# Kernel tuning notes

Measured on AMD Instinct MI355X. Metric: run time of the kernel, lower is better.

Reference implementation:

```python
import jax, jax.numpy as jnp
import numpy as np

N = 100000   # nodes
E = 250000   # directed edges
D = 300      # emb_dim
L = 5        # num_layers
BN_EPS = 1e-5
NUM_ATOM_TYPE, NUM_CHIRALITY_TAG = 120, 3
NUM_BOND_TYPE, NUM_BOND_DIR = 6, 3
SELF_LOOP_BOND = 4


def setup_inputs() -> dict:
    key = jax.random.key(0)
    ks = jax.random.split(key, 14)
    s = 0.02
    x = jnp.stack([jax.random.randint(ks[0], (N,), 0, NUM_ATOM_TYPE),
                   jax.random.randint(ks[1], (N,), 0, NUM_CHIRALITY_TAG)], axis=1)
    edge_index = jax.random.randint(ks[2], (2, E), 0, N)
    edge_attr = jnp.stack([jax.random.randint(ks[3], (E,), 0, 4),  # real bond types 0..3
                           jax.random.randint(ks[4], (E,), 0, NUM_BOND_DIR)], axis=1)
    x_emb1 = jax.random.normal(ks[5], (NUM_ATOM_TYPE, D), jnp.float32) * s
    x_emb2 = jax.random.normal(ks[6], (NUM_CHIRALITY_TAG, D), jnp.float32) * s
    ee1 = jax.random.normal(ks[7], (L, NUM_BOND_TYPE, D), jnp.float32) * s
    ee2 = jax.random.normal(ks[8], (L, NUM_BOND_DIR, D), jnp.float32) * s
    W1 = jax.random.normal(ks[9], (L, D, 2 * D), jnp.float32) * (1.0 / np.sqrt(D))
    b1 = jnp.zeros((L, 2 * D), jnp.float32)
    W2 = jax.random.normal(ks[10], (L, 2 * D, D), jnp.float32) * (1.0 / np.sqrt(2 * D))
    b2 = jnp.zeros((L, D), jnp.float32)
    eps = jnp.zeros((L,), jnp.float32)
    gamma = jnp.ones((L, D), jnp.float32)
    beta = jnp.zeros((L, D), jnp.float32)
    return {"x": x, "edge_index": edge_index, "edge_attr": edge_attr,
            "x_emb1": x_emb1, "x_emb2": x_emb2, "ee1": ee1, "ee2": ee2,
            "W1": W1, "b1": b1, "W2": W2, "b2": b2,
            "eps": eps, "gamma": gamma, "beta": beta}


def reference(x, edge_index, edge_attr, x_emb1, x_emb2, ee1, ee2,
              W1, b1, W2, b2, eps, gamma, beta):
    src, dst = edge_index[0], edge_index[1]
    n = x.shape[0]
    # Input atom embedding
    h = x_emb1[x[:, 0]] + x_emb2[x[:, 1]]  # [N, D]
    for l in range(L):
        # edge embedding gather (real edges)
        e_emb = ee1[l][edge_attr[:, 0]] + ee2[l][edge_attr[:, 1]]  # [E, D]
        # message: x_j + edge_emb, scatter-add to target nodes
        msg = h[src] + e_emb
        aggr = jax.ops.segment_sum(msg, dst, num_segments=n)  # [N, D]
        # self-loop edges: bond_type=4, bond_dir=0; x_j = h_i
        aggr = aggr + h + (ee1[l][SELF_LOOP_BOND] + ee2[l][0])
        # update: mlp((1 + eps) * aggr)
        z = (1.0 + eps[l]) * aggr
        z = jnp.maximum(z @ W1[l] + b1[l], 0.0) @ W2[l] + b2[l]
        # BatchNorm1d (training-mode batch statistics, dropout disabled)
        mean = z.mean(axis=0)
        var = z.var(axis=0)
        h = (z - mean) * jax.lax.rsqrt(var + BN_EPS) * gamma[l] + beta[l]
        if l < L - 1:
            h = jnp.maximum(h, 0.0)
    return h
```

## Files before the change

### kernel.cpp

```cpp
#include <hip/hip_runtime.h>
#include <cstdint>

#define NN 100000
#define NE 250000
#define MP 100096
#define MSTRIP 391
#define SCAN_B 256
#define NBLK ((NN + SCAN_B - 1) / SCAN_B)
#define NSLOT 32

using bf16x8 = __attribute__((ext_vector_type(8))) __bf16;
using f32x4v = __attribute__((ext_vector_type(4))) float;

__device__ __forceinline__ unsigned short f2bf(float f) {
  union { float f; uint32_t u; } v; v.f = f;
  uint32_t r = v.u + 0x7FFFu + ((v.u >> 16) & 1u);
  return (unsigned short)(r >> 16);
}
__device__ __forceinline__ float bf2f(unsigned short u) {
  union { uint32_t u; float f; } v; v.u = ((uint32_t)u) << 16;
  return v.f;
}

__device__ __forceinline__ void ld_lds16(const void* g, void* l) {
  __builtin_amdgcn_global_load_lds(
      (const __attribute__((address_space(1))) void*)g,
      (__attribute__((address_space(3))) void*)l, 16, 0, 0);
}

__global__ void prep_kernel(const float* __restrict__ W1, const float* __restrict__ W2,
                            const float* __restrict__ ee1, const float* __restrict__ ee2,
                            const float* __restrict__ b1, const float* __restrict__ b2, int l,
                            unsigned short* __restrict__ wt1, unsigned short* __restrict__ wt2,
                            float* __restrict__ combo, float* __restrict__ selfv,
                            float* __restrict__ b1p, float* __restrict__ b2p,
                            float* __restrict__ bnsum, float* __restrict__ bnsum2) {
  int i = blockIdx.x * 256 + threadIdx.x;
  if (i < 640 * 320) {
    int n = i / 320, k = i % 320;
    float v = (n < 600 && k < 300) ? W1[(size_t)l * 180000 + k * 600 + n] : 0.f;
    wt1[i] = f2bf(v); return;
  }
  i -= 640 * 320;
  if (i < 384 * 640) {
    int n = i / 640, k = i % 640;
    float v = (n < 300 && k < 600) ? W2[(size_t)l * 180000 + k * 300 + n] : 0.f;
    wt2[i] = f2bf(v); return;
  }
  i -= 384 * 640;
  if (i < 3600) {
    int idx = i / 300, d = i % 300;
    int a = idx / 3, b = idx % 3;
    combo[i] = ee1[l * 1800 + a * 300 + d] + ee2[l * 900 + b * 300 + d]; return;
  }
  i -= 3600;
  if (i < 300) { selfv[i] = ee1[l * 1800 + 4 * 300 + i] + ee2[l * 900 + i]; return; }
  i -= 300;
  if (i < 640) { b1p[i] = (i < 600) ? b1[l * 600 + i] : 0.f; return; }
  i -= 640;
  if (i < 384) { b2p[i] = (i < 300) ? b2[l * 300 + i] : 0.f; return; }
  i -= 384;
  if (i < NSLOT * 384) { bnsum[i] = 0.f; return; }
  i -= NSLOT * 384;
  if (i < NSLOT * 384) { bnsum2[i] = 0.f; return; }
}
#define PREP_TOT (640*320 + 384*640 + 3600 + 300 + 640 + 384 + 2*NSLOT*384)

__global__ void deg_kernel(const int* __restrict__ ei, int* __restrict__ deg) {
  int e = blockIdx.x * 256 + threadIdx.x;
  if (e >= NE) return;
  atomicAdd(&deg[ei[NE + e]], 1);
}

__global__ void scan1_kernel(const int* __restrict__ deg, int* __restrict__ off,
                             int* __restrict__ bsum) {
  __shared__ int tmp[SCAN_B];
  int b = blockIdx.x, t = threadIdx.x;
  int i = b * SCAN_B + t;
  int v = (i < NN) ? deg[i] : 0;
  tmp[t] = v;
  __syncthreads();
  for (int s = 1; s < SCAN_B; s <<= 1) {
    int a = (t >= s) ? tmp[t - s] : 0;
    __syncthreads();
    tmp[t] += a;
    __syncthreads();
  }
  if (i < NN) off[i] = tmp[t] - v;
  if (t == SCAN_B - 1) bsum[b] = tmp[t];
}
__global__ void scan2_kernel(int* __restrict__ bsum) {
  if (threadIdx.x == 0) {
    int acc = 0;
    for (int b = 0; b < NBLK; ++b) { int v = bsum[b]; bsum[b] = acc; acc += v; }
  }
}
__global__ void scan3_kernel(const int* __restrict__ bsum, int* __restrict__ off,
                             int* __restrict__ cursor) {
  int i = blockIdx.x * SCAN_B + threadIdx.x;
  if (i >= NN) return;
  int o = off[i] + bsum[blockIdx.x];
  off[i] = o;
  cursor[i] = o;
}

__global__ void fill_kernel(const int* __restrict__ ei, const int* __restrict__ ea,
                            int* __restrict__ cursor, int* __restrict__ list) {
  int e = blockIdx.x * 256 + threadIdx.x;
  if (e >= NE) return;
  int s = ei[e], d = ei[NE + e];
  int c = ea[2 * e] * 3 + ea[2 * e + 1];
  int p = atomicAdd(&cursor[d], 1);
  list[p] = s * 16 + c;
}

template <int MODE>
__global__ void gather_kernel(const unsigned short* __restrict__ zsrc,
                              const int* __restrict__ x, const float* __restrict__ e1,
                              const float* __restrict__ e2,
                              const float* __restrict__ bnA, const float* __restrict__ bnB,
                              const int* __restrict__ off, const int* __restrict__ deg,
                              const int* __restrict__ list,
                              const float* __restrict__ combo, const float* __restrict__ selfv,
                              const float* __restrict__ eps, int l,
                              unsigned short* __restrict__ abf) {
  int i = blockIdx.x * 256 + threadIdx.x;
  if (i >= NN * 75) return;
  int r = i / 75, q = i % 75;
  float4 a4, b4;
  if (MODE == 1) { a4 = ((const float4*)bnA)[q]; b4 = ((const float4*)bnB)[q]; }

  const ushort4* z4 = (const ushort4*)zsrc;
  const float4* c4 = (const float4*)combo;

  auto loadrow = [&](int s) -> float4 {
    float4 hv;
    if (MODE == 0) {
      float4 u = ((const float4*)(e1 + (size_t)x[2 * s] * 300))[q];
      float4 v = ((const float4*)(e2 + (size_t)x[2 * s + 1] * 300))[q];
      hv.x = u.x + v.x; hv.y = u.y + v.y; hv.z = u.z + v.z; hv.w = u.w + v.w;
    } else {
      ushort4 zv = z4[(size_t)s * 96 + q];
      hv.x = fmaxf(bf2f(zv.x) * a4.x + b4.x, 0.f);
      hv.y = fmaxf(bf2f(zv.y) * a4.y + b4.y, 0.f);
      hv.z = fmaxf(bf2f(zv.z) * a4.z + b4.z, 0.f);
      hv.w = fmaxf(bf2f(zv.w) * a4.w + b4.w, 0.f);
    }
    return hv;
  };

  float4 acc = loadrow(r);
  float4 sv = ((const float4*)selfv)[q];
  acc.x += sv.x; acc.y += sv.y; acc.z += sv.z; acc.w += sv.w;

  int p0 = off[r], dn = deg[r];
  for (int p = 0; p < dn; ++p) {
    int pk = list[p0 + p];
    int s = pk >> 4, c = pk & 15;
    float4 hv = loadrow(s);
    float4 cv = c4[c * 75 + q];
    acc.x += hv.x + cv.x; acc.y += hv.y + cv.y;
    acc.z += hv.z + cv.z; acc.w += hv.w + cv.w;
  }
  float sc = 1.f + eps[l];
  ushort4 o;
  o.x = f2bf(acc.x * sc); o.y = f2bf(acc.y * sc);
  o.z = f2bf(acc.z * sc); o.w = f2bf(acc.w * sc);
  *(ushort4*)(abf + (size_t)r * 320 + q * 4) = o;
}

template <int LDA, int LDB, int NS, int NT, bool RELU, bool OBF16, bool STATS>
__global__ __launch_bounds__(512, 4) void gemm_kernel(
    const unsigned short* __restrict__ A, const unsigned short* __restrict__ B,
    const float* __restrict__ bias, void* __restrict__ C, int K,
    float* __restrict__ bnsum, float* __restrict__ bnsum2) {
  __shared__ unsigned short As[2][256 * 32];
  __shared__ unsigned short Bs[2][128 * 32];
  const int tid = threadIdx.x;
  const int lane = tid & 63;
  const int w = tid >> 6;
  const int wr = w >> 1, wc = w & 1;
  const int l15 = lane & 15, l4 = lane >> 4;

  const int wid = blockIdx.x + gridDim.x * blockIdx.y;
  const int bmi = (wid & 7) + 8 * (wid / (8 * NT));
  const int ny  = (wid >> 3) % NT;
  if (bmi >= MSTRIP) return;
  const int bm = bmi * 256;
  const int bn = ny * 128;

  auto stage = [&](int buf, int kk) {
#pragma unroll
    for (int it = 0; it < 2; ++it) {
      int s = it * 512 + tid;
      int row = s >> 2, kbl = s & 3;
      int kbg = kbl ^ ((row >> 1) & 3);
      ld_lds16(A + (size_t)(bm + row) * LDA + kk + kbg * 8, &As[buf][s * 8]);
    }
    {
      int s = tid;
      int row = s >> 2, kbl = s & 3;
      int kbg = kbl ^ ((row >> 1) & 3);
      ld_lds16(B + (size_t)(bn + row) * LDB + kk + kbg * 8, &Bs[buf][s * 8]);
    }
  };

  f32x4v acc[4][4] = {};
  const int nt = K / 32;

  stage(0, 0);
  for (int t = 0; t < nt; ++t) {
    const int cur = t & 1;
    if (t + 1 < nt) {
      stage(cur ^ 1, (t + 1) * 32);
      asm volatile("s_waitcnt vmcnt(3)" ::: "memory");
    } else {
      asm volatile("s_waitcnt vmcnt(0)" ::: "memory");
    }
    __builtin_amdgcn_s_barrier();
    asm volatile("" ::: "memory");

    bf16x8 af[4], bfr[4];
#pragma unroll
    for (int mi = 0; mi < 4; ++mi) {
      int r = wr * 64 + mi * 16 + l15;
      int kb = l4 ^ ((r >> 1) & 3);
      af[mi] = *reinterpret_cast<const bf16x8*>(&As[cur][(r * 4 + kb) * 8]);
    }
#pragma unroll
    for (int ni = 0; ni < 4; ++ni) {
      int r = wc * 64 + ni * 16 + l15;
      int kb = l4 ^ ((r >> 1) & 3);
      bfr[ni] = *reinterpret_cast<const bf16x8*>(&Bs[cur][(r * 4 + kb) * 8]);
    }
#pragma unroll
    for (int mi = 0; mi < 4; ++mi)
#pragma unroll
      for (int ni = 0; ni < 4; ++ni)
        acc[mi][ni] = __builtin_amdgcn_mfma_f32_16x16x32_bf16(af[mi], bfr[ni], acc[mi][ni], 0, 0, 0);

    __builtin_amdgcn_s_barrier();
    asm volatile("" ::: "memory");
  }

  const int slot = wid & (NSLOT - 1);
#pragma unroll
  for (int ni = 0; ni < 4; ++ni) {
    int col = bn + wc * 64 + ni * 16 + l15;
    float bv = bias[col];
    float s = 0.f, s2 = 0.f;
#pragma unroll
    for (int mi = 0; mi < 4; ++mi) {
      int row0 = bm + wr * 64 + mi * 16 + (l4 << 2);
#pragma unroll
      for (int r = 0; r < 4; ++r) {
        float v = acc[mi][ni][r] + bv;
        if (RELU) v = fmaxf(v, 0.f);
        if (OBF16) ((unsigned short*)C)[(size_t)(row0 + r) * NS + col] = f2bf(v);
        else       ((float*)C)[(size_t)(row0 + r) * NS + col] = v;
        if (STATS && (row0 + r) < NN) { s += v; s2 += v * v; }
      }
    }
    if (STATS) {
      s  += __shfl_xor(s, 16);  s  += __shfl_xor(s, 32);
      s2 += __shfl_xor(s2, 16); s2 += __shfl_xor(s2, 32);
      if (l4 == 0) {
        atomicAdd(&bnsum[slot * 384 + col], s);
        atomicAdd(&bnsum2[slot * 384 + col], s2);
      }
    }
  }
}

__global__ void bnfinal_kernel(const float* __restrict__ bnsum, const float* __restrict__ bnsum2,
                               const float* __restrict__ gamma, const float* __restrict__ beta,
                               int l, float* __restrict__ Aout, float* __restrict__ Bout) {
  int c = threadIdx.x;
  if (c >= 300) return;
  float s = 0.f, s2 = 0.f;
  for (int k = 0; k < NSLOT; ++k) { s += bnsum[k * 384 + c]; s2 += bnsum2[k * 384 + c]; }
  float mean = s * (1.f / NN);
  float var = s2 * (1.f / NN) - mean * mean;
  var = fmaxf(var, 0.f);
  float inv = rsqrtf(var + 1e-5f);
  float a = gamma[l * 300 + c] * inv;
  Aout[c] = a;
  Bout[c] = beta[l * 300 + c] - mean * a;
}

__global__ void bnapply_kernel(const unsigned short* __restrict__ z, const float* __restrict__ Ain,
                               const float* __restrict__ Bin, float* __restrict__ out) {
  int i = blockIdx.x * 256 + threadIdx.x;
  if (i >= NN * 75) return;
  int r = i / 75, q = i % 75;
  ushort4 zv = ((const ushort4*)z)[(size_t)r * 96 + q];
  float4 a = ((const float4*)Ain)[q];
  float4 b = ((const float4*)Bin)[q];
  float4 o;
  o.x = bf2f(zv.x) * a.x + b.x; o.y = bf2f(zv.y) * a.y + b.y;
  o.z = bf2f(zv.z) * a.z + b.z; o.w = bf2f(zv.w) * a.w + b.w;
  ((float4*)out)[i] = o;
}

constexpr size_t OFF_Z    = 0;
constexpr size_t OFF_AB   = OFF_Z  + (size_t)MP * 384 * 2;
constexpr size_t OFF_Z1   = OFF_AB + (size_t)MP * 320 * 2;
constexpr size_t OFF_WT1  = OFF_Z1 + (size_t)MP * 640 * 2;
constexpr size_t OFF_WT2  = OFF_WT1 + 640 * 320 * 2;
constexpr size_t OFF_CMB  = OFF_WT2 + 384 * 640 * 2;
constexpr size_t OFF_SLF  = OFF_CMB + 14592;
constexpr size_t OFF_B1   = OFF_SLF + 1280;
constexpr size_t OFF_B2   = OFF_B1 + 2560;
constexpr size_t OFF_S1   = OFF_B2 + 1536;
constexpr size_t OFF_S2   = OFF_S1 + NSLOT * 384 * 4;
constexpr size_t OFF_BA   = OFF_S2 + NSLOT * 384 * 4;
constexpr size_t OFF_BB   = OFF_BA + 1536;
constexpr size_t OFF_DEG  = OFF_BB + 1536;
constexpr size_t OFF_OFFS = OFF_DEG + 400384;
constexpr size_t OFF_CUR  = OFF_OFFS + 400384;
constexpr size_t OFF_BS   = OFF_CUR + 400384;
constexpr size_t OFF_LIST = OFF_BS + 2048;

extern "C" void kernel_launch(void* const* d_in, const int* in_sizes, int n_in,
                              void* d_out, int out_size, void* d_ws, size_t ws_size,
                              hipStream_t stream) {
  const int*   x     = (const int*)d_in[0];
  const int*   ei    = (const int*)d_in[1];
  const int*   ea    = (const int*)d_in[2];
  const float* xe1   = (const float*)d_in[3];
  const float* xe2   = (const float*)d_in[4];
  const float* ee1   = (const float*)d_in[5];
  const float* ee2   = (const float*)d_in[6];
  const float* W1    = (const float*)d_in[7];
  const float* b1    = (const float*)d_in[8];
  const float* W2    = (const float*)d_in[9];
  const float* b2    = (const float*)d_in[10];
  const float* eps   = (const float*)d_in[11];
  const float* gamma = (const float*)d_in[12];
  const float* beta  = (const float*)d_in[13];

  char* ws = (char*)d_ws;
  unsigned short* zf    = (unsigned short*)(ws + OFF_Z);
  unsigned short* abf   = (unsigned short*)(ws + OFF_AB);
  unsigned short* z1    = (unsigned short*)(ws + OFF_Z1);
  unsigned short* wt1   = (unsigned short*)(ws + OFF_WT1);
  unsigned short* wt2   = (unsigned short*)(ws + OFF_WT2);
  float*          combo = (float*)(ws + OFF_CMB);
  float*          selfv = (float*)(ws + OFF_SLF);
  float*          b1p   = (float*)(ws + OFF_B1);
  float*          b2p   = (float*)(ws + OFF_B2);
  float*          bns   = (float*)(ws + OFF_S1);
  float*          bns2  = (float*)(ws + OFF_S2);
  float*          bnA   = (float*)(ws + OFF_BA);
  float*          bnB   = (float*)(ws + OFF_BB);
  int*            deg   = (int*)(ws + OFF_DEG);
  int*            offs  = (int*)(ws + OFF_OFFS);
  int*            cur   = (int*)(ws + OFF_CUR);
  int*            bsum  = (int*)(ws + OFF_BS);
  int*            list  = (int*)(ws + OFF_LIST);

  const int g_ew   = (NN * 75 + 255) / 256;
  const int g_e    = (NE + 255) / 256;
  const int g_prep = (PREP_TOT + 255) / 256;
  const int GX     = 392;

  hipMemsetAsync(abf, 0, (size_t)MP * 320 * 2, stream);
  hipMemsetAsync(deg, 0, NN * 4, stream);

  deg_kernel<<<g_e, 256, 0, stream>>>(ei, deg);
  scan1_kernel<<<NBLK, SCAN_B, 0, stream>>>(deg, offs, bsum);
  scan2_kernel<<<1, 64, 0, stream>>>(bsum);
  scan3_kernel<<<NBLK, SCAN_B, 0, stream>>>(bsum, offs, cur);
  fill_kernel<<<g_e, 256, 0, stream>>>(ei, ea, cur, list);

  for (int l = 0; l < 5; ++l) {
    prep_kernel<<<g_prep, 256, 0, stream>>>(W1, W2, ee1, ee2, b1, b2, l,
                                            wt1, wt2, combo, selfv, b1p, b2p, bns, bns2);
    if (l == 0)
      gather_kernel<0><<<g_ew, 256, 0, stream>>>(zf, x, xe1, xe2, bnA, bnB,
                                                 offs, deg, list, combo, selfv, eps, l, abf);
    else
      gather_kernel<1><<<g_ew, 256, 0, stream>>>(zf, x, xe1, xe2, bnA, bnB,
                                                 offs, deg, list, combo, selfv, eps, l, abf);
    gemm_kernel<320, 320, 640, 5, true, true, false><<<dim3(GX, 5), 512, 0, stream>>>(
        abf, wt1, b1p, (void*)z1, 320, bns, bns2);
    gemm_kernel<640, 640, 384, 3, false, true, true><<<dim3(GX, 3), 512, 0, stream>>>(
        z1, wt2, b2p, (void*)zf, 640, bns, bns2);
    bnfinal_kernel<<<1, 384, 0, stream>>>(bns, bns2, gamma, beta, l, bnA, bnB);
  }
  bnapply_kernel<<<g_ew, 256, 0, stream>>>(zf, bnA, bnB, (float*)d_out);
}
```

Before: 1.193 ms.

## Hoist per-layer weight prep out of loop and add narrow GEMM2 tail kernel

Weight transposition, bias padding and edge-embedding combos for all five layers are prepared in one launch before the layer loop, with per-layer BN accumulators zeroed up front. The second MLP GEMM now runs the generic kernel over two 128-wide column tiles and a new 64-wide kernel for the remaining columns. This cuts the padded work of the third 128-column tile and removes repeated prep launches, at the cost of more workspace and an extra launch per layer.

```diff
diff --git a/kernel.cpp b/kernel.cpp
--- a/kernel.cpp
+++ b/kernel.cpp
@@ -28,43 +28,46 @@
       (__attribute__((address_space(3))) void*)l, 16, 0, 0);
 }
 
+#define PER_L (640*320 + 384*640 + 3600 + 300 + 640 + 384)
+#define ZERO_N (5 * 2 * NSLOT * 384)
+#define PREP_TOT (5 * PER_L + ZERO_N)
 __global__ void prep_kernel(const float* __restrict__ W1, const float* __restrict__ W2,
                             const float* __restrict__ ee1, const float* __restrict__ ee2,
-                            const float* __restrict__ b1, const float* __restrict__ b2, int l,
+                            const float* __restrict__ b1, const float* __restrict__ b2,
                             unsigned short* __restrict__ wt1, unsigned short* __restrict__ wt2,
                             float* __restrict__ combo, float* __restrict__ selfv,
                             float* __restrict__ b1p, float* __restrict__ b2p,
-                            float* __restrict__ bnsum, float* __restrict__ bnsum2) {
+                            float* __restrict__ bnzero) {
   int i = blockIdx.x * 256 + threadIdx.x;
-  if (i < 640 * 320) {
-    int n = i / 320, k = i % 320;
-    float v = (n < 600 && k < 300) ? W1[(size_t)l * 180000 + k * 600 + n] : 0.f;
-    wt1[i] = f2bf(v); return;
-  }
-  i -= 640 * 320;
-  if (i < 384 * 640) {
-    int n = i / 640, k = i % 640;
-    float v = (n < 300 && k < 600) ? W2[(size_t)l * 180000 + k * 300 + n] : 0.f;
-    wt2[i] = f2bf(v); return;
-  }
-  i -= 384 * 640;
-  if (i < 3600) {
-    int idx = i / 300, d = i % 300;
-    int a = idx / 3, b = idx % 3;
-    combo[i] = ee1[l * 1800 + a * 300 + d] + ee2[l * 900 + b * 300 + d]; return;
-  }
-  i -= 3600;
-  if (i < 300) { selfv[i] = ee1[l * 1800 + 4 * 300 + i] + ee2[l * 900 + i]; return; }
-  i -= 300;
-  if (i < 640) { b1p[i] = (i < 600) ? b1[l * 600 + i] : 0.f; return; }
-  i -= 640;
-  if (i < 384) { b2p[i] = (i < 300) ? b2[l * 300 + i] : 0.f; return; }
-  i -= 384;
-  if (i < NSLOT * 384) { bnsum[i] = 0.f; return; }
-  i -= NSLOT * 384;
-  if (i < NSLOT * 384) { bnsum2[i] = 0.f; return; }
-}
-#define PREP_TOT (640*320 + 384*640 + 3600 + 300 + 640 + 384 + 2*NSLOT*384)
+  if (i < 5 * PER_L) {
+    int l = i / PER_L, j = i - l * PER_L;
+    if (j < 640 * 320) {
+      int n = j / 320, k = j % 320;
+      float v = (n < 600 && k < 300) ? W1[(size_t)l * 180000 + k * 600 + n] : 0.f;
+      wt1[l * 204800 + j] = f2bf(v); return;
+    }
+    j -= 640 * 320;
+    if (j < 384 * 640) {
+      int n = j / 640, k = j % 640;
+      float v = (n < 300 && k < 600) ? W2[(size_t)l * 180000 + k * 300 + n] : 0.f;
+      wt2[l * 245760 + j] = f2bf(v); return;
+    }
+    j -= 384 * 640;
+    if (j < 3600) {
+      int idx = j / 300, d = j % 300;
+      int a = idx / 3, b = idx % 3;
+      combo[l * 3600 + j] = ee1[l * 1800 + a * 300 + d] + ee2[l * 900 + b * 300 + d]; return;
+    }
+    j -= 3600;
+    if (j < 300) { selfv[l * 300 + j] = ee1[l * 1800 + 4 * 300 + j] + ee2[l * 900 + j]; return; }
+    j -= 300;
+    if (j < 640) { b1p[l * 640 + j] = (j < 600) ? b1[l * 600 + j] : 0.f; return; }
+    j -= 640;
+    b2p[l * 384 + j] = (j < 300) ? b2[l * 300 + j] : 0.f; return;
+  }
+  i -= 5 * PER_L;
+  if (i < ZERO_N) bnzero[i] = 0.f;
+}
 
 __global__ void deg_kernel(const int* __restrict__ ei, int* __restrict__ deg) {
   int e = blockIdx.x * 256 + threadIdx.x;
@@ -272,6 +275,98 @@
   }
 }
 
+__global__ __launch_bounds__(256, 2) void gemm2_narrow_kernel(
+    const unsigned short* __restrict__ A, const unsigned short* __restrict__ B,
+    const float* __restrict__ bias, unsigned short* __restrict__ C,
+    float* __restrict__ bnsum, float* __restrict__ bnsum2) {
+  __shared__ unsigned short As[2][256 * 32];
+  __shared__ unsigned short Bs[2][64 * 32];
+  const int tid = threadIdx.x;
+  const int lane = tid & 63;
+  const int w = tid >> 6;
+  const int l15 = lane & 15, l4 = lane >> 4;
+  const int bmi = blockIdx.x;
+  if (bmi >= MSTRIP) return;
+  const int bm = bmi * 256;
+  const int bn = 256;
+
+  auto stage = [&](int buf, int kk) {
+#pragma unroll
+    for (int it = 0; it < 4; ++it) {
+      int s = it * 256 + tid;
+      int row = s >> 2, kbl = s & 3;
+      int kbg = kbl ^ ((row >> 1) & 3);
+      ld_lds16(A + (size_t)(bm + row) * 640 + kk + kbg * 8, &As[buf][s * 8]);
+    }
+    {
+      int s = tid;
+      int row = s >> 2, kbl = s & 3;
+      int kbg = kbl ^ ((row >> 1) & 3);
+      ld_lds16(B + (size_t)(bn + row) * 640 + kk + kbg * 8, &Bs[buf][s * 8]);
+    }
+  };
+
+  f32x4v acc[4][4] = {};
+  stage(0, 0);
+  for (int t = 0; t < 20; ++t) {
+    const int cur = t & 1;
+    if (t + 1 < 20) {
+      stage(cur ^ 1, (t + 1) * 32);
+      asm volatile("s_waitcnt vmcnt(5)" ::: "memory");
+    } else {
+      asm volatile("s_waitcnt vmcnt(0)" ::: "memory");
+    }
+    __builtin_amdgcn_s_barrier();
+    asm volatile("" ::: "memory");
+
+    bf16x8 af[4], bfr[4];
+#pragma unroll
+    for (int mi = 0; mi < 4; ++mi) {
+      int r = w * 64 + mi * 16 + l15;
+      int kb = l4 ^ ((r >> 1) & 3);
+      af[mi] = *reinterpret_cast<const bf16x8*>(&As[cur][(r * 4 + kb) * 8]);
+    }
+#pragma unroll
+    for (int ni = 0; ni < 4; ++ni) {
+      int r = ni * 16 + l15;
+      int kb = l4 ^ ((r >> 1) & 3);
+      bfr[ni] = *reinterpret_cast<const bf16x8*>(&Bs[cur][(r * 4 + kb) * 8]);
+    }
+#pragma unroll
+    for (int mi = 0; mi < 4; ++mi)
+#pragma unroll
+      for (int ni = 0; ni < 4; ++ni)
+        acc[mi][ni] = __builtin_amdgcn_mfma_f32_16x16x32_bf16(af[mi], bfr[ni], acc[mi][ni], 0, 0, 0);
+
+    __builtin_amdgcn_s_barrier();
+    asm volatile("" ::: "memory");
+  }
+
+  const int slot = bmi & (NSLOT - 1);
+#pragma unroll
+  for (int ni = 0; ni < 4; ++ni) {
+    int col = bn + ni * 16 + l15;
+    float bv = bias[col];
+    float s = 0.f, s2 = 0.f;
+#pragma unroll
+    for (int mi = 0; mi < 4; ++mi) {
+      int row0 = bm + w * 64 + mi * 16 + (l4 << 2);
+#pragma unroll
+      for (int r = 0; r < 4; ++r) {
+        float v = acc[mi][ni][r] + bv;
+        C[(size_t)(row0 + r) * 384 + col] = f2bf(v);
+        if ((row0 + r) < NN) { s += v; s2 += v * v; }
+      }
+    }
+    s  += __shfl_xor(s, 16);  s  += __shfl_xor(s, 32);
+    s2 += __shfl_xor(s2, 16); s2 += __shfl_xor(s2, 32);
+    if (l4 == 0) {
+      atomicAdd(&bnsum[slot * 384 + col], s);
+      atomicAdd(&bnsum2[slot * 384 + col], s2);
+    }
+  }
+}
+
 __global__ void bnfinal_kernel(const float* __restrict__ bnsum, const float* __restrict__ bnsum2,
                                const float* __restrict__ gamma, const float* __restrict__ beta,
                                int l, float* __restrict__ Aout, float* __restrict__ Bout) {
@@ -306,14 +401,14 @@
 constexpr size_t OFF_AB   = OFF_Z  + (size_t)MP * 384 * 2;
 constexpr size_t OFF_Z1   = OFF_AB + (size_t)MP * 320 * 2;
 constexpr size_t OFF_WT1  = OFF_Z1 + (size_t)MP * 640 * 2;
-constexpr size_t OFF_WT2  = OFF_WT1 + 640 * 320 * 2;
-constexpr size_t OFF_CMB  = OFF_WT2 + 384 * 640 * 2;
-constexpr size_t OFF_SLF  = OFF_CMB + 14592;
-constexpr size_t OFF_B1   = OFF_SLF + 1280;
-constexpr size_t OFF_B2   = OFF_B1 + 2560;
-constexpr size_t OFF_S1   = OFF_B2 + 1536;
-constexpr size_t OFF_S2   = OFF_S1 + NSLOT * 384 * 4;
-constexpr size_t OFF_BA   = OFF_S2 + NSLOT * 384 * 4;
+constexpr size_t OFF_WT2  = OFF_WT1 + (size_t)5 * 204800 * 2;
+constexpr size_t OFF_CMB  = OFF_WT2 + (size_t)5 * 245760 * 2;
+constexpr size_t OFF_SLF  = OFF_CMB + 5 * 3600 * 4;
+constexpr size_t OFF_B1   = OFF_SLF + 5 * 300 * 4 + 144;
+constexpr size_t OFF_B2   = OFF_B1 + 5 * 640 * 4;
+constexpr size_t OFF_S1   = OFF_B2 + 5 * 384 * 4;
+constexpr size_t OFF_S2   = OFF_S1 + (size_t)5 * NSLOT * 384 * 4;
+constexpr size_t OFF_BA   = OFF_S2 + (size_t)5 * NSLOT * 384 * 4;
 constexpr size_t OFF_BB   = OFF_BA + 1536;
 constexpr size_t OFF_DEG  = OFF_BB + 1536;
 constexpr size_t OFF_OFFS = OFF_DEG + 400384;
@@ -367,6 +462,9 @@
   hipMemsetAsync(abf, 0, (size_t)MP * 320 * 2, stream);
   hipMemsetAsync(deg, 0, NN * 4, stream);
 
+  prep_kernel<<<g_prep, 256, 0, stream>>>(W1, W2, ee1, ee2, b1, b2,
+                                          wt1, wt2, combo, selfv, b1p, b2p, bns);
+
   deg_kernel<<<g_e, 256, 0, stream>>>(ei, deg);
   scan1_kernel<<<NBLK, SCAN_B, 0, stream>>>(deg, offs, bsum);
   scan2_kernel<<<1, 64, 0, stream>>>(bsum);
@@ -374,19 +472,23 @@
   fill_kernel<<<g_e, 256, 0, stream>>>(ei, ea, cur, list);
 
   for (int l = 0; l < 5; ++l) {
-    prep_kernel<<<g_prep, 256, 0, stream>>>(W1, W2, ee1, ee2, b1, b2, l,
-                                            wt1, wt2, combo, selfv, b1p, b2p, bns, bns2);
+    float* bns_l  = bns  + (size_t)l * NSLOT * 384;
+    float* bns2_l = bns2 + (size_t)l * NSLOT * 384;
     if (l == 0)
       gather_kernel<0><<<g_ew, 256, 0, stream>>>(zf, x, xe1, xe2, bnA, bnB,
-                                                 offs, deg, list, combo, selfv, eps, l, abf);
+                                                 offs, deg, list, combo + l * 3600,
+                                                 selfv + l * 300, eps, l, abf);
     else
       gather_kernel<1><<<g_ew, 256, 0, stream>>>(zf, x, xe1, xe2, bnA, bnB,
-                                                 offs, deg, list, combo, selfv, eps, l, abf);
+                                                 offs, deg, list, combo + l * 3600,
+                                                 selfv + l * 300, eps, l, abf);
     gemm_kernel<320, 320, 640, 5, true, true, false><<<dim3(GX, 5), 512, 0, stream>>>(
-        abf, wt1, b1p, (void*)z1, 320, bns, bns2);
-    gemm_kernel<640, 640, 384, 3, false, true, true><<<dim3(GX, 3), 512, 0, stream>>>(
-        z1, wt2, b2p, (void*)zf, 640, bns, bns2);
-    bnfinal_kernel<<<1, 384, 0, stream>>>(bns, bns2, gamma, beta, l, bnA, bnB);
+        abf, wt1 + (size_t)l * 204800, b1p + l * 640, (void*)z1, 320, bns_l, bns2_l);
+    gemm_kernel<640, 640, 384, 2, false, true, true><<<dim3(GX, 2), 512, 0, stream>>>(
+        z1, wt2 + (size_t)l * 245760, b2p + l * 384, (void*)zf, 640, bns_l, bns2_l);
+    gemm2_narrow_kernel<<<GX, 256, 0, stream>>>(
+        z1, wt2 + (size_t)l * 245760, b2p + l * 384, zf, bns_l, bns2_l);
+    bnfinal_kernel<<<1, 384, 0, stream>>>(bns_l, bns2_l, gamma, beta, l, bnA, bnB);
   }
   bnapply_kernel<<<g_ew, 256, 0, stream>>>(zf, bnA, bnB, (float*)d_out);
 }
```

Measured after the change: 1.253 ms. +5.0%, slower.

## Hoist per-layer weight prep into one launch and widen gather to 8 columns

Applied to the files above, without the earlier changes.

Moves weight transposition and bias/embedding prep for all five layers into one kernel launched before the loop. Per-layer buffers, including separate BN stat accumulators, keep the layers independent. The gather kernel now handles 8 columns per thread using padded 304-wide embedding and combo tables, which halves the thread count and issues wider loads. This removes four launches and their serialization, at the cost of more workspace.

```diff
diff --git a/kernel.cpp b/kernel.cpp
--- a/kernel.cpp
+++ b/kernel.cpp
@@ -11,6 +11,7 @@
 
 using bf16x8 = __attribute__((ext_vector_type(8))) __bf16;
 using f32x4v = __attribute__((ext_vector_type(4))) float;
+using u16x8 = __attribute__((ext_vector_type(8))) unsigned short;
 
 __device__ __forceinline__ unsigned short f2bf(float f) {
   union { float f; uint32_t u; } v; v.f = f;
@@ -28,43 +29,66 @@
       (__attribute__((address_space(3))) void*)l, 16, 0, 0);
 }
 
+#define PER_L (640*320 + 384*640 + 12*304 + 304 + 640 + 384)
+#define GLOB_N (120*304 + 3*304 + 2*384 + 5*2*NSLOT*384)
+#define PREP_TOT (5 * PER_L + GLOB_N)
 __global__ void prep_kernel(const float* __restrict__ W1, const float* __restrict__ W2,
                             const float* __restrict__ ee1, const float* __restrict__ ee2,
-                            const float* __restrict__ b1, const float* __restrict__ b2, int l,
+                            const float* __restrict__ b1, const float* __restrict__ b2,
+                            const float* __restrict__ xe1, const float* __restrict__ xe2,
                             unsigned short* __restrict__ wt1, unsigned short* __restrict__ wt2,
                             float* __restrict__ combo, float* __restrict__ selfv,
                             float* __restrict__ b1p, float* __restrict__ b2p,
-                            float* __restrict__ bnsum, float* __restrict__ bnsum2) {
+                            float* __restrict__ e1p, float* __restrict__ e2p,
+                            float* __restrict__ bnAB, float* __restrict__ bnacc) {
   int i = blockIdx.x * 256 + threadIdx.x;
-  if (i < 640 * 320) {
-    int n = i / 320, k = i % 320;
-    float v = (n < 600 && k < 300) ? W1[(size_t)l * 180000 + k * 600 + n] : 0.f;
-    wt1[i] = f2bf(v); return;
-  }
-  i -= 640 * 320;
-  if (i < 384 * 640) {
-    int n = i / 640, k = i % 640;
-    float v = (n < 300 && k < 600) ? W2[(size_t)l * 180000 + k * 300 + n] : 0.f;
-    wt2[i] = f2bf(v); return;
-  }
-  i -= 384 * 640;
-  if (i < 3600) {
-    int idx = i / 300, d = i % 300;
-    int a = idx / 3, b = idx % 3;
-    combo[i] = ee1[l * 1800 + a * 300 + d] + ee2[l * 900 + b * 300 + d]; return;
-  }
-  i -= 3600;
-  if (i < 300) { selfv[i] = ee1[l * 1800 + 4 * 300 + i] + ee2[l * 900 + i]; return; }
-  i -= 300;
-  if (i < 640) { b1p[i] = (i < 600) ? b1[l * 600 + i] : 0.f; return; }
-  i -= 640;
-  if (i < 384) { b2p[i] = (i < 300) ? b2[l * 300 + i] : 0.f; return; }
-  i -= 384;
-  if (i < NSLOT * 384) { bnsum[i] = 0.f; return; }
-  i -= NSLOT * 384;
-  if (i < NSLOT * 384) { bnsum2[i] = 0.f; return; }
-}
-#define PREP_TOT (640*320 + 384*640 + 3600 + 300 + 640 + 384 + 2*NSLOT*384)
+  if (i < 5 * PER_L) {
+    int l = i / PER_L, j = i - l * PER_L;
+    if (j < 640 * 320) {
+      int n = j / 320, k = j % 320;
+      float v = (n < 600 && k < 300) ? W1[(size_t)l * 180000 + k * 600 + n] : 0.f;
+      wt1[l * 204800 + j] = f2bf(v); return;
+    }
+    j -= 640 * 320;
+    if (j < 384 * 640) {
+      int n = j / 640, k = j % 640;
+      float v = (n < 300 && k < 600) ? W2[(size_t)l * 180000 + k * 300 + n] : 0.f;
+      wt2[l * 245760 + j] = f2bf(v); return;
+    }
+    j -= 384 * 640;
+    if (j < 12 * 304) {
+      int idx = j / 304, d = j % 304;
+      int a = idx / 3, b = idx % 3;
+      combo[l * 3648 + j] = (d < 300)
+          ? ee1[l * 1800 + a * 300 + d] + ee2[l * 900 + b * 300 + d] : 0.f;
+      return;
+    }
+    j -= 12 * 304;
+    if (j < 304) {
+      selfv[l * 304 + j] = (j < 300)
+          ? ee1[l * 1800 + 4 * 300 + j] + ee2[l * 900 + j] : 0.f;
+      return;
+    }
+    j -= 304;
+    if (j < 640) { b1p[l * 640 + j] = (j < 600) ? b1[l * 600 + j] : 0.f; return; }
+    j -= 640;
+    b2p[l * 384 + j] = (j < 300) ? b2[l * 300 + j] : 0.f; return;
+  }
+  i -= 5 * PER_L;
+  if (i < 120 * 304) {
+    int n = i / 304, d = i % 304;
+    e1p[i] = (d < 300) ? xe1[n * 300 + d] : 0.f; return;
+  }
+  i -= 120 * 304;
+  if (i < 3 * 304) {
+    int n = i / 304, d = i % 304;
+    e2p[i] = (d < 300) ? xe2[n * 300 + d] : 0.f; return;
+  }
+  i -= 3 * 304;
+  if (i < 2 * 384) { bnAB[i] = 0.f; return; }
+  i -= 2 * 384;
+  if (i < 5 * 2 * NSLOT * 384) bnacc[i] = 0.f;
+}
 
 __global__ void deg_kernel(const int* __restrict__ ei, int* __restrict__ deg) {
   int e = blockIdx.x * 256 + threadIdx.x;
@@ -116,8 +140,8 @@
 
 template <int MODE>
 __global__ void gather_kernel(const unsigned short* __restrict__ zsrc,
-                              const int* __restrict__ x, const float* __restrict__ e1,
-                              const float* __restrict__ e2,
+                              const int* __restrict__ x, const float* __restrict__ e1p,
+                              const float* __restrict__ e2p,
                               const float* __restrict__ bnA, const float* __restrict__ bnB,
                               const int* __restrict__ off, const int* __restrict__ deg,
                               const int* __restrict__ list,
@@ -125,48 +149,66 @@
                               const float* __restrict__ eps, int l,
                               unsigned short* __restrict__ abf) {
   int i = blockIdx.x * 256 + threadIdx.x;
-  if (i >= NN * 75) return;
-  int r = i / 75, q = i % 75;
-  float4 a4, b4;
-  if (MODE == 1) { a4 = ((const float4*)bnA)[q]; b4 = ((const float4*)bnB)[q]; }
-
-  const ushort4* z4 = (const ushort4*)zsrc;
-  const float4* c4 = (const float4*)combo;
-
-  auto loadrow = [&](int s) -> float4 {
-    float4 hv;
+  if (i >= NN * 38) return;
+  int r = i / 38, qc = i % 38;
+  const int cb = qc * 8;
+
+  float4 a0, a1, b0, b1;
+  if (MODE == 1) {
+    a0 = *(const float4*)(bnA + cb); a1 = *(const float4*)(bnA + cb + 4);
+    b0 = *(const float4*)(bnB + cb); b1 = *(const float4*)(bnB + cb + 4);
+  }
+
+  auto loadrow = [&](int s, float4& oL, float4& oH) {
     if (MODE == 0) {
-      float4 u = ((const float4*)(e1 + (size_t)x[2 * s] * 300))[q];
-      float4 v = ((const float4*)(e2 + (size_t)x[2 * s + 1] * 300))[q];
-      hv.x = u.x + v.x; hv.y = u.y + v.y; hv.z = u.z + v.z; hv.w = u.w + v.w;
+      const float* p1 = e1p + (size_t)x[2 * s] * 304 + cb;
+      const float* p2 = e2p + (size_t)x[2 * s + 1] * 304 + cb;
+      float4 u0 = *(const float4*)p1, u1 = *(const float4*)(p1 + 4);
+      float4 v0 = *(const float4*)p2, v1 = *(const float4*)(p2 + 4);
+      oL.x = u0.x + v0.x; oL.y = u0.y + v0.y; oL.z = u0.z + v0.z; oL.w = u0.w + v0.w;
+      oH.x = u1.x + v1.x; oH.y = u1.y + v1.y; oH.z = u1.z + v1.z; oH.w = u1.w + v1.w;
     } else {
-      ushort4 zv = z4[(size_t)s * 96 + q];
-      hv.x = fmaxf(bf2f(zv.x) * a4.x + b4.x, 0.f);
-      hv.y = fmaxf(bf2f(zv.y) * a4.y + b4.y, 0.f);
-      hv.z = fmaxf(bf2f(zv.z) * a4.z + b4.z, 0.f);
-      hv.w = fmaxf(bf2f(zv.w) * a4.w + b4.w, 0.f);
-    }
-    return hv;
+      u16x8 zv = *reinterpret_cast<const u16x8*>(zsrc + (size_t)s * 384 + cb);
+      oL.x = fmaxf(bf2f(zv[0]) * a0.x + b0.x, 0.f);
+      oL.y = fmaxf(bf2f(zv[1]) * a0.y + b0.y, 0.f);
+      oL.z = fmaxf(bf2f(zv[2]) * a0.z + b0.z, 0.f);
+      oL.w = fmaxf(bf2f(zv[3]) * a0.w + b0.w, 0.f);
+      oH.x = fmaxf(bf2f(zv[4]) * a1.x + b1.x, 0.f);
+      oH.y = fmaxf(bf2f(zv[5]) * a1.y + b1.y, 0.f);
+      oH.z = fmaxf(bf2f(zv[6]) * a1.z + b1.z, 0.f);
+      oH.w = fmaxf(bf2f(zv[7]) * a1.w + b1.w, 0.f);
+    }
   };
 
-  float4 acc = loadrow(r);
-  float4 sv = ((const float4*)selfv)[q];
-  acc.x += sv.x; acc.y += sv.y; acc.z += sv.z; acc.w += sv.w;
+  float4 accL, accH;
+  loadrow(r, accL, accH);
+  {
+    float4 s0 = *(const float4*)(selfv + cb), s1 = *(const float4*)(selfv + cb + 4);
+    accL.x += s0.x; accL.y += s0.y; accL.z += s0.z; accL.w += s0.w;
+    accH.x += s1.x; accH.y += s1.y; accH.z += s1.z; accH.w += s1.w;
+  }
 
   int p0 = off[r], dn = deg[r];
   for (int p = 0; p < dn; ++p) {
     int pk = list[p0 + p];
     int s = pk >> 4, c = pk & 15;
-    float4 hv = loadrow(s);
-    float4 cv = c4[c * 75 + q];
-    acc.x += hv.x + cv.x; acc.y += hv.y + cv.y;
-    acc.z += hv.z + cv.z; acc.w += hv.w + cv.w;
-  }
+    float4 hL, hH;
+    loadrow(s, hL, hH);
+    const float* cp = combo + c * 304 + cb;
+    float4 c0 = *(const float4*)cp, c1 = *(const float4*)(cp + 4);
+    accL.x += hL.x + c0.x; accL.y += hL.y + c0.y;
+    accL.z += hL.z + c0.z; accL.w += hL.w + c0.w;
+    accH.x += hH.x + c1.x; accH.y += hH.y + c1.y;
+    accH.z += hH.z + c1.z; accH.w += hH.w + c1.w;
+  }
+
   float sc = 1.f + eps[l];
-  ushort4 o;
-  o.x = f2bf(acc.x * sc); o.y = f2bf(acc.y * sc);
-  o.z = f2bf(acc.z * sc); o.w = f2bf(acc.w * sc);
-  *(ushort4*)(abf + (size_t)r * 320 + q * 4) = o;
+  u16x8 o;
+  o[0] = f2bf(accL.x * sc); o[1] = f2bf(accL.y * sc);
+  o[2] = f2bf(accL.z * sc); o[3] = f2bf(accL.w * sc);
+  o[4] = f2bf(accH.x * sc); o[5] = f2bf(accH.y * sc);
+  o[6] = f2bf(accH.z * sc); o[7] = f2bf(accH.w * sc);
+  *reinterpret_cast<u16x8*>(abf + (size_t)r * 320 + cb) = o;
 }
 
 template <int LDA, int LDB, int NS, int NT, bool RELU, bool OBF16, bool STATS>
@@ -303,17 +345,19 @@
 }
 
 constexpr size_t OFF_Z    = 0;
-constexpr size_t OFF_AB   = OFF_Z  + (size_t)MP * 384 * 2;
-constexpr size_t OFF_Z1   = OFF_AB + (size_t)MP * 320 * 2;
-constexpr size_t OFF_WT1  = OFF_Z1 + (size_t)MP * 640 * 2;
-constexpr size_t OFF_WT2  = OFF_WT1 + 640 * 320 * 2;
-constexpr size_t OFF_CMB  = OFF_WT2 + 384 * 640 * 2;
-constexpr size_t OFF_SLF  = OFF_CMB + 14592;
-constexpr size_t OFF_B1   = OFF_SLF + 1280;
-constexpr size_t OFF_B2   = OFF_B1 + 2560;
-constexpr size_t OFF_S1   = OFF_B2 + 1536;
-constexpr size_t OFF_S2   = OFF_S1 + NSLOT * 384 * 4;
-constexpr size_t OFF_BA   = OFF_S2 + NSLOT * 384 * 4;
+constexpr size_t OFF_AB   = OFF_Z   + (size_t)MP * 384 * 2;
+constexpr size_t OFF_Z1   = OFF_AB  + (size_t)MP * 320 * 2;
+constexpr size_t OFF_WT1  = OFF_Z1  + (size_t)MP * 640 * 2;
+constexpr size_t OFF_WT2  = OFF_WT1 + (size_t)5 * 204800 * 2;
+constexpr size_t OFF_CMB  = OFF_WT2 + (size_t)5 * 245760 * 2;
+constexpr size_t OFF_SLF  = OFF_CMB + 5 * 3648 * 4;
+constexpr size_t OFF_E1P  = OFF_SLF + 5 * 304 * 4;
+constexpr size_t OFF_E2P  = OFF_E1P + 120 * 304 * 4;
+constexpr size_t OFF_B1   = OFF_E2P + 3 * 304 * 4;
+constexpr size_t OFF_B2   = OFF_B1  + 5 * 640 * 4;
+constexpr size_t OFF_S1   = OFF_B2  + 5 * 384 * 4;
+constexpr size_t OFF_S2   = OFF_S1  + (size_t)5 * NSLOT * 384 * 4;
+constexpr size_t OFF_BA   = OFF_S2  + (size_t)5 * NSLOT * 384 * 4;
 constexpr size_t OFF_BB   = OFF_BA + 1536;
 constexpr size_t OFF_DEG  = OFF_BB + 1536;
 constexpr size_t OFF_OFFS = OFF_DEG + 400384;
@@ -347,6 +391,8 @@
   unsigned short* wt2   = (unsigned short*)(ws + OFF_WT2);
   float*          combo = (float*)(ws + OFF_CMB);
   float*          selfv = (float*)(ws + OFF_SLF);
+  float*          e1p   = (float*)(ws + OFF_E1P);
+  float*          e2p   = (float*)(ws + OFF_E2P);
   float*          b1p   = (float*)(ws + OFF_B1);
   float*          b2p   = (float*)(ws + OFF_B2);
   float*          bns   = (float*)(ws + OFF_S1);
@@ -359,6 +405,7 @@
   int*            bsum  = (int*)(ws + OFF_BS);
   int*            list  = (int*)(ws + OFF_LIST);
 
+  const int g_g    = (NN * 38 + 255) / 256;
   const int g_ew   = (NN * 75 + 255) / 256;
   const int g_e    = (NE + 255) / 256;
   const int g_prep = (PREP_TOT + 255) / 256;
@@ -366,6 +413,10 @@
 
   hipMemsetAsync(abf, 0, (size_t)MP * 320 * 2, stream);
   hipMemsetAsync(deg, 0, NN * 4, stream);
+
+  prep_kernel<<<g_prep, 256, 0, stream>>>(W1, W2, ee1, ee2, b1, b2, xe1, xe2,
+                                          wt1, wt2, combo, selfv, b1p, b2p,
+                                          e1p, e2p, bnA, bns);
 
   deg_kernel<<<g_e, 256, 0, stream>>>(ei, deg);
   scan1_kernel<<<NBLK, SCAN_B, 0, stream>>>(deg, offs, bsum);
@@ -374,19 +425,21 @@
   fill_kernel<<<g_e, 256, 0, stream>>>(ei, ea, cur, list);
 
   for (int l = 0; l < 5; ++l) {
-    prep_kernel<<<g_prep, 256, 0, stream>>>(W1, W2, ee1, ee2, b1, b2, l,
-                                            wt1, wt2, combo, selfv, b1p, b2p, bns, bns2);
+    float* bns_l  = bns  + (size_t)l * NSLOT * 384;
+    float* bns2_l = bns2 + (size_t)l * NSLOT * 384;
     if (l == 0)
-      gather_kernel<0><<<g_ew, 256, 0, stream>>>(zf, x, xe1, xe2, bnA, bnB,
-                                                 offs, deg, list, combo, selfv, eps, l, abf);
+      gather_kernel<0><<<g_g, 256, 0, stream>>>(zf, x, e1p, e2p, bnA, bnB,
+                                                offs, deg, list, combo + l * 3648,
+                                                selfv + l * 304, eps, l, abf);
     else
-      gather_kernel<1><<<g_ew, 256, 0, stream>>>(zf, x, xe1, xe2, bnA, bnB,
-                                                 offs, deg, list, combo, selfv, eps, l, abf);
+      gather_kernel<1><<<g_g, 256, 0, stream>>>(zf, x, e1p, e2p, bnA, bnB,
+                                                offs, deg, list, combo + l * 3648,
+                                                selfv + l * 304, eps, l, abf);
     gemm_kernel<320, 320, 640, 5, true, true, false><<<dim3(GX, 5), 512, 0, stream>>>(
-        abf, wt1, b1p, (void*)z1, 320, bns, bns2);
+        abf, wt1 + (size_t)l * 204800, b1p + l * 640, (void*)z1, 320, bns_l, bns2_l);
     gemm_kernel<640, 640, 384, 3, false, true, true><<<dim3(GX, 3), 512, 0, stream>>>(
-        z1, wt2, b2p, (void*)zf, 640, bns, bns2);
-    bnfinal_kernel<<<1, 384, 0, stream>>>(bns, bns2, gamma, beta, l, bnA, bnB);
+        z1, wt2 + (size_t)l * 245760, b2p + l * 384, (void*)zf, 640, bns_l, bns2_l);
+    bnfinal_kernel<<<1, 384, 0, stream>>>(bns_l, bns2_l, gamma, beta, l, bnA, bnB);
   }
   bnapply_kernel<<<g_ew, 256, 0, stream>>>(zf, bnA, bnB, (float*)d_out);
 }
```

After: 1.139 ms. -4.6%, faster.
